# Kernel optimization log

Measured on AMD Instinct MI355X. Metric: run time of the kernel, lower is better.

The kernel has to match this reference:

```python
import jax, jax.numpy as jnp
import numpy as np

U, SI, TI = 100000, 50000, 40000
D = 64
B = 8192
NNZ_S, NNZ_T = 3_200_000, 2_560_000
P_DROP = 0.2


def setup_inputs() -> dict:
    key = jax.random.key(0)
    ks = iter(jax.random.split(key, 32))
    nxt = lambda: next(ks)
    emb = lambda n: (jax.random.normal(nxt(), (n, D), jnp.float32) * 0.1)
    keep = lambda n: jax.random.bernoulli(nxt(), 1.0 - P_DROP, (n,)).astype(jnp.float32) / (1.0 - P_DROP)
    inp = {}
    inp['user'] = jax.random.randint(nxt(), (B,), 0, U, jnp.int32)
    inp['source_pos_item'] = jax.random.randint(nxt(), (B,), 0, SI, jnp.int32)
    inp['source_neg_item'] = jax.random.randint(nxt(), (B,), 0, SI, jnp.int32)
    inp['target_pos_item'] = jax.random.randint(nxt(), (B,), 0, TI, jnp.int32)
    inp['target_neg_item'] = jax.random.randint(nxt(), (B,), 0, TI, jnp.int32)
    inp['mask_s'] = jax.random.bernoulli(nxt(), 0.5, (B,))
    inp['mask_t'] = jax.random.bernoulli(nxt(), 0.5, (B,))
    inp['su_int'] = emb(U); inp['si_int'] = emb(SI)
    inp['tu_int'] = emb(U); inp['ti_int'] = emb(TI)
    inp['su_pop'] = emb(U); inp['si_pop'] = emb(SI)
    inp['tu_pop'] = emb(U); inp['ti_pop'] = emb(TI)
    Ns, Nt = U + SI, U + TI
    inp['s_rows'] = jax.random.randint(nxt(), (NNZ_S,), 0, Ns, jnp.int32)
    inp['s_cols'] = jax.random.randint(nxt(), (NNZ_S,), 0, Ns, jnp.int32)
    inp['s_vals'] = jax.random.uniform(nxt(), (NNZ_S,), jnp.float32, 0.0, 0.02)
    inp['t_rows'] = jax.random.randint(nxt(), (NNZ_T,), 0, Nt, jnp.int32)
    inp['t_cols'] = jax.random.randint(nxt(), (NNZ_T,), 0, Nt, jnp.int32)
    inp['t_vals'] = jax.random.uniform(nxt(), (NNZ_T,), jnp.float32, 0.0, 0.02)
    inp['drop_s_int'] = keep(NNZ_S); inp['drop_t_int'] = keep(NNZ_T)
    inp['drop_s_pop'] = keep(NNZ_S); inp['drop_t_pop'] = keep(NNZ_T)
    return inp


def _lightgcn(emb, rows, cols, vals, n_users):
    # 1-layer LightGCN: out = mean([e0, A @ e0]) ; A given as COO (rows, cols, vals)
    agg = jax.ops.segment_sum(vals[:, None] * emb[cols], rows, num_segments=emb.shape[0])
    out = 0.5 * (emb + agg)
    return out[:n_users], out[n_users:]


def _bpr(p, n):
    return -jnp.mean(jax.nn.log_sigmoid(p - n))


def _mask_bpr(p, n, m):
    return -jnp.mean(m.astype(p.dtype) * jax.nn.log_sigmoid(p - n))


def _masked_l1(a, b, idx):
    # L1Loss(mean) over rows selected by unique(idx); membership mask avoids jnp.unique
    m = jnp.zeros((a.shape[0],), bool).at[idx].set(True)
    cnt = jnp.maximum(m.sum(), 1).astype(a.dtype)
    return jnp.sum(jnp.abs(a - b) * m[:, None]) / (cnt * a.shape[1])


def reference(user, source_pos_item, source_neg_item, target_pos_item, target_neg_item,
              mask_s, mask_t,
              su_int, si_int, tu_int, ti_int, su_pop, si_pop, tu_pop, ti_pop,
              s_rows, s_cols, s_vals, t_rows, t_cols, t_vals,
              drop_s_int, drop_t_int, drop_s_pop, drop_t_pop):
    # int factor
    us_i, is_i = _lightgcn(jnp.concatenate([su_int, si_int]), s_rows, s_cols, s_vals * drop_s_int, U)
    ut_i, it_i = _lightgcn(jnp.concatenate([tu_int, ti_int]), t_rows, t_cols, t_vals * drop_t_int, U)
    # pop factor
    us_p, is_p = _lightgcn(jnp.concatenate([su_pop, si_pop]), s_rows, s_cols, s_vals * drop_s_pop, U)
    ut_p, it_p = _lightgcn(jnp.concatenate([tu_pop, ti_pop]), t_rows, t_cols, t_vals * drop_t_pop, U)

    dot = lambda ue, ie, u, i: jnp.sum(ue[u] * ie[i], axis=1)
    sp_i = dot(us_i, is_i, user, source_pos_item); sn_i = dot(us_i, is_i, user, source_neg_item)
    sp_p = dot(us_p, is_p, user, source_pos_item); sn_p = dot(us_p, is_p, user, source_neg_item)
    tp_i = dot(ut_i, it_i, user, target_pos_item); tn_i = dot(ut_i, it_i, user, target_neg_item)
    tp_p = dot(ut_p, it_p, user, target_pos_item); tn_p = dot(ut_p, it_p, user, target_neg_item)

    loss_int_s = _mask_bpr(sp_i, sn_i, mask_s)
    loss_pop_s = _mask_bpr(sn_p, sp_p, mask_s) + _mask_bpr(sp_p, sn_p, ~mask_s)
    loss_int_t = _mask_bpr(tp_i, tn_i, mask_t)
    loss_pop_t = _mask_bpr(tn_p, tp_p, mask_t) + _mask_bpr(tp_p, tn_p, ~mask_t)
    loss_total_s = _bpr(sp_i + sp_p, sn_i + sn_p)
    loss_total_t = _bpr(tp_i + tp_p, tn_i + tn_p)

    item_all_s = jnp.concatenate([source_pos_item, source_neg_item])
    item_all_t = jnp.concatenate([target_pos_item, target_neg_item])
    dis_loss = (_masked_l1(su_int, su_pop, user) + _masked_l1(si_int, si_pop, item_all_s)
                + _masked_l1(tu_int, tu_pop, user) + _masked_l1(ti_int, ti_pop, item_all_t))

    loss = (loss_total_s + loss_total_t
            + 0.1 * (loss_int_s + loss_int_t)
            + 0.1 * (loss_pop_s + loss_pop_t)
            - 0.01 * dis_loss)
    return loss
```

## Files before the change

### kernel.cpp

```cpp
#include <hip/hip_runtime.h>
#include <math.h>

constexpr int U_N = 100000;
constexpr int SI_N = 50000;
constexpr int TI_N = 40000;
constexpr int D = 64;
constexpr int B = 8192;
constexpr int NS = U_N + SI_N;
constexpr int NT = U_N + TI_N;
constexpr int SLOTS = 3 * B;
constexpr int CAP = 64;
constexpr int OVCAP = 4096;
constexpr int NROWS_ALL = U_N + SI_N + TI_N;
constexpr int NCHUNK = (NROWS_ALL + 63) / 64;

__device__ __forceinline__ float wave_sum(float x) {
#pragma unroll
  for (int m = 32; m; m >>= 1) x += __shfl_xor(x, m, 64);
  return x;
}

__device__ __forceinline__ float softplus_f(float z) {
  return fmaxf(z, 0.f) + log1pf(expf(-fabsf(z)));
}

__global__ __launch_bounds__(256) void k_init(
    const int* __restrict__ user, const int* __restrict__ spos, const int* __restrict__ sneg,
    const int* __restrict__ tpos, const int* __restrict__ tneg,
    int* __restrict__ map_s, int* __restrict__ map_t,
    const unsigned char* __restrict__ m, int* __restrict__ det) {
  if (blockIdx.x < 96) {
    int t = blockIdx.x * blockDim.x + threadIdx.x;
    if (t < B) {
      int u = user[t];
      map_s[u] = t;
      map_t[u] = t;
    } else if (t < 2 * B) {
      int b = t - B;
      map_s[U_N + spos[b]] = t;
      map_t[U_N + tpos[b]] = t;
    } else {
      int b = t - 2 * B;
      map_s[U_N + sneg[b]] = t;
      map_t[U_N + tneg[b]] = t;
    }
    return;
  }
  int t = threadIdx.x;
  int cb = 0, cc = 0;
  for (int i = t; i < B; i += 256) {
    unsigned char v = m[i];
    if ((i & 3) && v) cb++;
    if (v > 1) cc++;
  }
#pragma unroll
  for (int off = 32; off; off >>= 1) {
    cb += __shfl_xor(cb, off, 64);
    cc += __shfl_xor(cc, off, 64);
  }
  __shared__ int sb[4], sc[4];
  if ((t & 63) == 0) { sb[t >> 6] = cb; sc[t >> 6] = cc; }
  __syncthreads();
  if (t == 0) {
    det[0] = sb[0] + sb[1] + sb[2] + sb[3];
    det[1] = sc[0] + sc[1] + sc[2] + sc[3];
  }
}

__global__ __launch_bounds__(256) void k_compact2(
    const int* __restrict__ s_rows, const int* __restrict__ t_rows,
    const int* __restrict__ map_s, const int* __restrict__ map_t,
    int* __restrict__ cnt_s, int* __restrict__ cnt_t,
    int* __restrict__ bucket_s, int* __restrict__ bucket_t,
    int* __restrict__ ovcnt_s, int* __restrict__ ovcnt_t,
    int* __restrict__ ov_s, int* __restrict__ ov_t, int nnz_s, int nnz_t) {
  int e = blockIdx.x * 256 + threadIdx.x;
  const int* rows;
  const int* map;
  int* cnt;
  int* bucket;
  int* ovcnt;
  int* ov;
  if (e < nnz_s) {
    rows = s_rows; map = map_s; cnt = cnt_s; bucket = bucket_s; ovcnt = ovcnt_s; ov = ov_s;
  } else {
    e -= nnz_s;
    if (e >= nnz_t) return;
    rows = t_rows; map = map_t; cnt = cnt_t; bucket = bucket_t; ovcnt = ovcnt_t; ov = ov_t;
  }
  int slot = map[rows[e]];
  if (slot < 0) return;
  int pos = atomicAdd(&cnt[slot], 1);
  if (pos < CAP) {
    bucket[slot * CAP + pos] = e;
  } else {
    int o = atomicAdd(ovcnt, 1);
    if (o < OVCAP) { ov[2 * o] = slot; ov[2 * o + 1] = e; }
  }
}

__device__ __forceinline__ void accum_slot(
    int s, int lane,
    const int* __restrict__ cols, const float* __restrict__ vals,
    const float* __restrict__ di, const float* __restrict__ dp,
    const int* __restrict__ cnt, const int* __restrict__ bucket,
    const int* __restrict__ ovcnt, const int* __restrict__ ov,
    const float* __restrict__ eu_i, const float* __restrict__ ei_i,
    const float* __restrict__ eu_p, const float* __restrict__ ei_p,
    float* __restrict__ aggA, float* __restrict__ aggB) {
  int m = min(cnt[s], CAP);
  int g = lane >> 4, sub = lane & 15;
  int c = 0;
  float wi = 0.f, wp = 0.f;
  if (lane < m) {
    int e = bucket[s * CAP + lane];
    c = cols[e];
    float v = vals[e];
    wi = v * di[e];
    wp = v * dp[e];
  }
  float aIx = 0, aIy = 0, aIz = 0, aIw = 0;
  float aPx = 0, aPy = 0, aPz = 0, aPw = 0;
  for (int k = 0; k < m; k += 16) {
    int i0 = k + g, i1 = k + 4 + g, i2 = k + 8 + g, i3 = k + 12 + g;
    int c0 = __shfl(c, i0, 64), c1 = __shfl(c, i1, 64);
    int c2 = __shfl(c, i2, 64), c3 = __shfl(c, i3, 64);
    float wi0 = __shfl(wi, i0, 64), wi1 = __shfl(wi, i1, 64);
    float wi2 = __shfl(wi, i2, 64), wi3 = __shfl(wi, i3, 64);
    float wp0 = __shfl(wp, i0, 64), wp1 = __shfl(wp, i1, 64);
    float wp2 = __shfl(wp, i2, 64), wp3 = __shfl(wp, i3, 64);
    const float* bi0 = (c0 < U_N) ? (eu_i + (size_t)c0 * D) : (ei_i + (size_t)(c0 - U_N) * D);
    const float* bi1 = (c1 < U_N) ? (eu_i + (size_t)c1 * D) : (ei_i + (size_t)(c1 - U_N) * D);
    const float* bi2 = (c2 < U_N) ? (eu_i + (size_t)c2 * D) : (ei_i + (size_t)(c2 - U_N) * D);
    const float* bi3 = (c3 < U_N) ? (eu_i + (size_t)c3 * D) : (ei_i + (size_t)(c3 - U_N) * D);
    const float* bp0 = (c0 < U_N) ? (eu_p + (size_t)c0 * D) : (ei_p + (size_t)(c0 - U_N) * D);
    const float* bp1 = (c1 < U_N) ? (eu_p + (size_t)c1 * D) : (ei_p + (size_t)(c1 - U_N) * D);
    const float* bp2 = (c2 < U_N) ? (eu_p + (size_t)c2 * D) : (ei_p + (size_t)(c2 - U_N) * D);
    const float* bp3 = (c3 < U_N) ? (eu_p + (size_t)c3 * D) : (ei_p + (size_t)(c3 - U_N) * D);
    float4 vI0 = *(const float4*)(bi0 + 4 * sub);
    float4 vI1 = *(const float4*)(bi1 + 4 * sub);
    float4 vI2 = *(const float4*)(bi2 + 4 * sub);
    float4 vI3 = *(const float4*)(bi3 + 4 * sub);
    float4 vP0 = *(const float4*)(bp0 + 4 * sub);
    float4 vP1 = *(const float4*)(bp1 + 4 * sub);
    float4 vP2 = *(const float4*)(bp2 + 4 * sub);
    float4 vP3 = *(const float4*)(bp3 + 4 * sub);
    aIx = fmaf(wi0, vI0.x, aIx); aIy = fmaf(wi0, vI0.y, aIy);
    aIz = fmaf(wi0, vI0.z, aIz); aIw = fmaf(wi0, vI0.w, aIw);
    aIx = fmaf(wi1, vI1.x, aIx); aIy = fmaf(wi1, vI1.y, aIy);
    aIz = fmaf(wi1, vI1.z, aIz); aIw = fmaf(wi1, vI1.w, aIw);
    aIx = fmaf(wi2, vI2.x, aIx); aIy = fmaf(wi2, vI2.y, aIy);
    aIz = fmaf(wi2, vI2.z, aIz); aIw = fmaf(wi2, vI2.w, aIw);
    aIx = fmaf(wi3, vI3.x, aIx); aIy = fmaf(wi3, vI3.y, aIy);
    aIz = fmaf(wi3, vI3.z, aIz); aIw = fmaf(wi3, vI3.w, aIw);
    aPx = fmaf(wp0, vP0.x, aPx); aPy = fmaf(wp0, vP0.y, aPy);
    aPz = fmaf(wp0, vP0.z, aPz); aPw = fmaf(wp0, vP0.w, aPw);
    aPx = fmaf(wp1, vP1.x, aPx); aPy = fmaf(wp1, vP1.y, aPy);
    aPz = fmaf(wp1, vP1.z, aPz); aPw = fmaf(wp1, vP1.w, aPw);
    aPx = fmaf(wp2, vP2.x, aPx); aPy = fmaf(wp2, vP2.y, aPy);
    aPz = fmaf(wp2, vP2.z, aPz); aPw = fmaf(wp2, vP2.w, aPw);
    aPx = fmaf(wp3, vP3.x, aPx); aPy = fmaf(wp3, vP3.y, aPy);
    aPz = fmaf(wp3, vP3.z, aPz); aPw = fmaf(wp3, vP3.w, aPw);
  }
#define XRED(x) x += __shfl_xor(x, 16, 64); x += __shfl_xor(x, 32, 64);
  XRED(aIx) XRED(aIy) XRED(aIz) XRED(aIw)
  XRED(aPx) XRED(aPy) XRED(aPz) XRED(aPw)
#undef XRED
  int nov = min(*ovcnt, OVCAP);
  for (int i = 0; i < nov; ++i) {
    if (ov[2 * i] == s) {
      int e = ov[2 * i + 1];
      int cc = cols[e];
      float v = vals[e];
      float wwi = v * di[e], wwp = v * dp[e];
      const float* bi = (cc < U_N) ? (eu_i + (size_t)cc * D) : (ei_i + (size_t)(cc - U_N) * D);
      const float* bp = (cc < U_N) ? (eu_p + (size_t)cc * D) : (ei_p + (size_t)(cc - U_N) * D);
      if (lane < 16) {
        float4 vI = *(const float4*)(bi + 4 * sub);
        float4 vP = *(const float4*)(bp + 4 * sub);
        aIx = fmaf(wwi, vI.x, aIx); aIy = fmaf(wwi, vI.y, aIy);
        aIz = fmaf(wwi, vI.z, aIz); aIw = fmaf(wwi, vI.w, aIw);
        aPx = fmaf(wwp, vP.x, aPx); aPy = fmaf(wwp, vP.y, aPy);
        aPz = fmaf(wwp, vP.z, aPz); aPw = fmaf(wwp, vP.w, aPw);
      }
    }
  }
  if (lane < 16) {
    *(float4*)(aggA + (size_t)s * D + 4 * sub) = make_float4(aIx, aIy, aIz, aIw);
    *(float4*)(aggB + (size_t)s * D + 4 * sub) = make_float4(aPx, aPy, aPz, aPw);
  }
}

__global__ __launch_bounds__(256) void k_accum_pair(
    const int* __restrict__ s_cols, const float* __restrict__ s_vals,
    const float* __restrict__ dsi, const float* __restrict__ dsp,
    const int* __restrict__ t_cols, const float* __restrict__ t_vals,
    const float* __restrict__ dti, const float* __restrict__ dtp,
    const int* __restrict__ cnt_s, const int* __restrict__ bucket_s,
    const int* __restrict__ ovcnt_s, const int* __restrict__ ov_s,
    const int* __restrict__ cnt_t, const int* __restrict__ bucket_t,
    const int* __restrict__ ovcnt_t, const int* __restrict__ ov_t,
    const float* __restrict__ su_i, const float* __restrict__ si_i,
    const float* __restrict__ su_p, const float* __restrict__ si_p,
    const float* __restrict__ tu_i, const float* __restrict__ ti_i,
    const float* __restrict__ tu_p, const float* __restrict__ ti_p,
    float* __restrict__ aggSA, float* __restrict__ aggSB,
    float* __restrict__ aggTA, float* __restrict__ aggTB) {
  int lane = threadIdx.x & 63;
  int sg = (blockIdx.x * 256 + threadIdx.x) >> 6;
  if (sg >= 2 * SLOTS) return;
  if (sg < SLOTS) {
    accum_slot(sg, lane, s_cols, s_vals, dsi, dsp, cnt_s, bucket_s, ovcnt_s, ov_s,
               su_i, si_i, su_p, si_p, aggSA, aggSB);
  } else {
    accum_slot(sg - SLOTS, lane, t_cols, t_vals, dti, dtp, cnt_t, bucket_t, ovcnt_t, ov_t,
               tu_i, ti_i, tu_p, ti_p, aggTA, aggTB);
  }
}

__global__ __launch_bounds__(256) void k_dots_loss(
    const int* __restrict__ user,
    const int* __restrict__ spos, const int* __restrict__ sneg,
    const int* __restrict__ tpos, const int* __restrict__ tneg,
    const unsigned char* __restrict__ ms8, const unsigned char* __restrict__ mt8,
    const int* __restrict__ det,
    const float* __restrict__ su_i, const float* __restrict__ si_i,
    const float* __restrict__ su_p, const float* __restrict__ si_p,
    const float* __restrict__ tu_i, const float* __restrict__ ti_i,
    const float* __restrict__ tu_p, const float* __restrict__ ti_p,
    const int* __restrict__ map_s, const int* __restrict__ map_t,
    const float* __restrict__ aggSA, const float* __restrict__ aggSB,
    const float* __restrict__ aggTA, const float* __restrict__ aggTB,
    float* __restrict__ acc) {
  int lane = threadIdx.x & 63;
  int b = (blockIdx.x * blockDim.x + threadIdx.x) >> 6;
  float contrib = 0.f;
  if (b < B) {
    int u = user[b];
    int ps = spos[b], ns = sneg[b], pt = tpos[b], nt = tneg[b];
    int sus = map_s[u], sps = map_s[U_N + ps], sns = map_s[U_N + ns];
    int sut = map_t[u], spt = map_t[U_N + pt], snt = map_t[U_N + nt];
    float oui = su_i[(size_t)u * D + lane] + aggSA[(size_t)sus * D + lane];
    float oup = su_p[(size_t)u * D + lane] + aggSB[(size_t)sus * D + lane];
    float opi = si_i[(size_t)ps * D + lane] + aggSA[(size_t)sps * D + lane];
    float opp = si_p[(size_t)ps * D + lane] + aggSB[(size_t)sps * D + lane];
    float oni = si_i[(size_t)ns * D + lane] + aggSA[(size_t)sns * D + lane];
    float onp = si_p[(size_t)ns * D + lane] + aggSB[(size_t)sns * D + lane];
    float spi = 0.25f * wave_sum(oui * opi);
    float sni = 0.25f * wave_sum(oui * oni);
    float spp = 0.25f * wave_sum(oup * opp);
    float snp = 0.25f * wave_sum(oup * onp);
    float tui = tu_i[(size_t)u * D + lane] + aggTA[(size_t)sut * D + lane];
    float tup = tu_p[(size_t)u * D + lane] + aggTB[(size_t)sut * D + lane];
    float tpi_ = ti_i[(size_t)pt * D + lane] + aggTA[(size_t)spt * D + lane];
    float tpp_ = ti_p[(size_t)pt * D + lane] + aggTB[(size_t)spt * D + lane];
    float tni_ = ti_i[(size_t)nt * D + lane] + aggTA[(size_t)snt * D + lane];
    float tnp_ = ti_p[(size_t)nt * D + lane] + aggTB[(size_t)snt * D + lane];
    float tpi = 0.25f * wave_sum(tui * tpi_);
    float tni = 0.25f * wave_sum(tui * tni_);
    float tpp = 0.25f * wave_sum(tup * tpp_);
    float tnp = 0.25f * wave_sum(tup * tnp_);
    int db = det[0], dc = det[1];
    float ms, mt;
    if (dc > 100) {
      ms = (((const float*)ms8)[b] != 0.f) ? 1.f : 0.f;
      mt = (((const float*)mt8)[b] != 0.f) ? 1.f : 0.f;
    } else if (db > 100) {
      ms = ms8[b] ? 1.f : 0.f;
      mt = mt8[b] ? 1.f : 0.f;
    } else {
      ms = ((const int*)ms8)[b] ? 1.f : 0.f;
      mt = ((const int*)mt8)[b] ? 1.f : 0.f;
    }
    float l_int_s = ms * softplus_f(sni - spi);
    float l_pop_s = ms * softplus_f(spp - snp) + (1.f - ms) * softplus_f(snp - spp);
    float l_tot_s = softplus_f((sni + snp) - (spi + spp));
    float l_int_t = mt * softplus_f(tni - tpi);
    float l_pop_t = mt * softplus_f(tpp - tnp) + (1.f - mt) * softplus_f(tnp - tpp);
    float l_tot_t = softplus_f((tni + tnp) - (tpi + tpp));
    contrib = (l_tot_s + l_tot_t + 0.1f * (l_int_s + l_int_t) +
               0.1f * (l_pop_s + l_pop_t)) * (1.f / (float)B);
  }
  __shared__ float wsum_[4];
  if (lane == 0) wsum_[threadIdx.x >> 6] = contrib;
  __syncthreads();
  if (threadIdx.x == 0) atomicAdd(&acc[0], wsum_[0] + wsum_[1] + wsum_[2] + wsum_[3]);
}

__global__ __launch_bounds__(256) void k_l1_final(
    const float* __restrict__ su_i, const float* __restrict__ su_p,
    const float* __restrict__ tu_i, const float* __restrict__ tu_p,
    const float* __restrict__ si_i, const float* __restrict__ si_p,
    const float* __restrict__ ti_i, const float* __restrict__ ti_p,
    const int* __restrict__ map_s, const int* __restrict__ map_t,
    float* __restrict__ acc, int* __restrict__ done_ctr,
    float* __restrict__ out) {
  int lane = threadIdx.x & 63;
  int wave = (blockIdx.x * blockDim.x + threadIdx.x) >> 6;
  int nwaves = (gridDim.x * blockDim.x) >> 6;
  float a1 = 0.f, a2 = 0.f, a3 = 0.f, a4 = 0.f;
  float c5 = 0.f, c6 = 0.f, c7 = 0.f;
  for (int ch = wave; ch < NCHUNK; ch += nwaves) {
    int r0 = ch * 64;
    int r = r0 + lane;
    int flag = -1;
    if (r < NROWS_ALL) flag = (r < NS) ? map_s[r] : map_t[r - SI_N];
    bool valid = flag >= 0;
    unsigned long long m0 = __ballot(valid && r < U_N);
    unsigned long long m1 = __ballot(valid && r >= U_N && r < NS);
    unsigned long long m2 = __ballot(valid && r >= NS);
    if (lane == 0) {
      c5 += (float)__popcll(m0);
      c6 += (float)__popcll(m1);
      c7 += (float)__popcll(m2);
    }
    unsigned long long mm = m0 | m1 | m2;
    while (mm) {
      int bit = __ffsll((unsigned long long)mm) - 1;
      mm &= mm - 1;
      int rr = r0 + bit;
      if (rr < U_N) {
        size_t o = (size_t)rr * D + lane;
        a1 += fabsf(su_i[o] - su_p[o]);
        a3 += fabsf(tu_i[o] - tu_p[o]);
      } else if (rr < NS) {
        size_t o = (size_t)(rr - U_N) * D + lane;
        a2 += fabsf(si_i[o] - si_p[o]);
      } else {
        size_t o = (size_t)(rr - NS) * D + lane;
        a4 += fabsf(ti_i[o] - ti_p[o]);
      }
    }
  }
  a1 = wave_sum(a1);
  a2 = wave_sum(a2);
  a3 = wave_sum(a3);
  a4 = wave_sum(a4);
  __shared__ float sb[4][8];
  if (lane == 0) {
    int w = threadIdx.x >> 6;
    sb[w][0] = a1; sb[w][1] = a2; sb[w][2] = a3; sb[w][3] = a4;
    sb[w][4] = c5; sb[w][5] = c6; sb[w][6] = c7;
  }
  __syncthreads();
  int t = threadIdx.x;
  if (t < 7) {
    float v = sb[0][t] + sb[1][t] + sb[2][t] + sb[3][t];
    atomicAdd(&acc[1 + t], v);
  }
  __syncthreads();
  if (t == 0) {
    __threadfence();
    int old = atomicAdd(done_ctr, 1);
    if (old == (int)gridDim.x - 1) {
      float a0 = atomicAdd(&acc[0], 0.f);
      float n1 = atomicAdd(&acc[1], 0.f);
      float n2 = atomicAdd(&acc[2], 0.f);
      float n3 = atomicAdd(&acc[3], 0.f);
      float n4 = atomicAdd(&acc[4], 0.f);
      float cu = fmaxf(atomicAdd(&acc[5], 0.f), 1.f);
      float cs = fmaxf(atomicAdd(&acc[6], 0.f), 1.f);
      float ct = fmaxf(atomicAdd(&acc[7], 0.f), 1.f);
      float dis = n1 / (cu * (float)D) + n2 / (cs * (float)D) +
                  n3 / (cu * (float)D) + n4 / (ct * (float)D);
      out[0] = a0 - 0.01f * dis;
    }
  }
}

extern "C" void kernel_launch(void* const* d_in, const int* in_sizes, int n_in,
                              void* d_out, int out_size, void* d_ws, size_t ws_size,
                              hipStream_t stream) {
  const int* user = (const int*)d_in[0];
  const int* spos = (const int*)d_in[1];
  const int* sneg = (const int*)d_in[2];
  const int* tpos = (const int*)d_in[3];
  const int* tneg = (const int*)d_in[4];
  const unsigned char* mask_s = (const unsigned char*)d_in[5];
  const unsigned char* mask_t = (const unsigned char*)d_in[6];
  const float* su_int = (const float*)d_in[7];
  const float* si_int = (const float*)d_in[8];
  const float* tu_int = (const float*)d_in[9];
  const float* ti_int = (const float*)d_in[10];
  const float* su_pop = (const float*)d_in[11];
  const float* si_pop = (const float*)d_in[12];
  const float* tu_pop = (const float*)d_in[13];
  const float* ti_pop = (const float*)d_in[14];
  const int* s_rows = (const int*)d_in[15];
  const int* s_cols = (const int*)d_in[16];
  const float* s_vals = (const float*)d_in[17];
  const int* t_rows = (const int*)d_in[18];
  const int* t_cols = (const int*)d_in[19];
  const float* t_vals = (const float*)d_in[20];
  const float* drop_s_int = (const float*)d_in[21];
  const float* drop_t_int = (const float*)d_in[22];
  const float* drop_s_pop = (const float*)d_in[23];
  const float* drop_t_pop = (const float*)d_in[24];
  const int nnz_s = in_sizes[15];
  const int nnz_t = in_sizes[18];

  float* acc = (float*)d_ws;
  int* done_ctr = (int*)(acc + 16);
  int* det = done_ctr + 1;
  int* ovcnt_s = det + 2;
  int* ovcnt_t = ovcnt_s + 1;
  int* cnt_s = ovcnt_t + 1;
  int* cnt_t = cnt_s + SLOTS;
  int* map_s = cnt_t + SLOTS;
  int* map_t = map_s + NS;
  int* ov_s = map_t + NT;
  int* ov_t = ov_s + 2 * OVCAP;
  int* bucket_s = ov_t + 2 * OVCAP;
  int* bucket_t = bucket_s + SLOTS * CAP;
  float* aggSA = (float*)(bucket_t + SLOTS * CAP);
  float* aggSB = aggSA + (size_t)SLOTS * D;
  float* aggTA = aggSB + (size_t)SLOTS * D;
  float* aggTB = aggTA + (size_t)SLOTS * D;

  hipMemsetAsync(acc, 0, (size_t)(16 + 1 + 2 + 2 + 2 * SLOTS) * sizeof(int), stream);
  hipMemsetAsync(map_s, 0xFF, (size_t)(NS + NT) * sizeof(int), stream);

  k_init<<<97, 256, 0, stream>>>(user, spos, sneg, tpos, tneg, map_s, map_t, mask_s, det);

  k_compact2<<<(nnz_s + nnz_t + 255) / 256, 256, 0, stream>>>(
      s_rows, t_rows, map_s, map_t, cnt_s, cnt_t, bucket_s, bucket_t,
      ovcnt_s, ovcnt_t, ov_s, ov_t, nnz_s, nnz_t);

  k_accum_pair<<<2 * SLOTS / 4, 256, 0, stream>>>(
      s_cols, s_vals, drop_s_int, drop_s_pop, t_cols, t_vals, drop_t_int, drop_t_pop,
      cnt_s, bucket_s, ovcnt_s, ov_s, cnt_t, bucket_t, ovcnt_t, ov_t,
      su_int, si_int, su_pop, si_pop, tu_int, ti_int, tu_pop, ti_pop,
      aggSA, aggSB, aggTA, aggTB);

  k_dots_loss<<<(B + 3) / 4, 256, 0, stream>>>(
      user, spos, sneg, tpos, tneg, mask_s, mask_t, det,
      su_int, si_int, su_pop, si_pop, tu_int, ti_int, tu_pop, ti_pop,
      map_s, map_t, aggSA, aggSB, aggTA, aggTB, acc);

  k_l1_final<<<768, 256, 0, stream>>>(su_int, su_pop, tu_int, tu_pop,
                                      si_int, si_pop, ti_int, ti_pop,
                                      map_s, map_t, acc, done_ctr, (float*)d_out);
}
```

Measured before the change: 483.8 us.

## Pack col and weights into buckets, shrink CAP, merge dots and L1 kernels

The compaction kernel now gathers each edge's column, value and both dropout weights once and stores them as an int4 in the bucket. This removes the dependent indirect loads through the edge index in the accumulation kernel. CAP drops from 64 to 48, trading more overflow-list traffic for smaller buckets. The dot-product/loss and L1 kernels are fused into one launch that shares a done-counter finalization, removing one kernel launch. Compact writes 16 bytes per kept edge instead of 4, and all edges beyond 48 per row now go through the serial overflow scan.

```diff
diff --git a/kernel.cpp b/kernel.cpp
--- a/kernel.cpp
+++ b/kernel.cpp
@@ -9,10 +9,12 @@
 constexpr int NS = U_N + SI_N;
 constexpr int NT = U_N + TI_N;
 constexpr int SLOTS = 3 * B;
-constexpr int CAP = 64;
+constexpr int CAP = 48;
 constexpr int OVCAP = 4096;
 constexpr int NROWS_ALL = U_N + SI_N + TI_N;
 constexpr int NCHUNK = (NROWS_ALL + 63) / 64;
+constexpr int DOTS_BLOCKS = B / 4;
+constexpr int L1_BLOCKS = 768;
 
 __device__ __forceinline__ float wave_sum(float x) {
 #pragma unroll
@@ -68,56 +70,72 @@
 }
 
 __global__ __launch_bounds__(256) void k_compact2(
-    const int* __restrict__ s_rows, const int* __restrict__ t_rows,
+    const int* __restrict__ s_rows, const int* __restrict__ s_cols,
+    const float* __restrict__ s_vals,
+    const float* __restrict__ dsi, const float* __restrict__ dsp,
+    const int* __restrict__ t_rows, const int* __restrict__ t_cols,
+    const float* __restrict__ t_vals,
+    const float* __restrict__ dti, const float* __restrict__ dtp,
     const int* __restrict__ map_s, const int* __restrict__ map_t,
     int* __restrict__ cnt_s, int* __restrict__ cnt_t,
-    int* __restrict__ bucket_s, int* __restrict__ bucket_t,
+    int4* __restrict__ bucket_s, int4* __restrict__ bucket_t,
     int* __restrict__ ovcnt_s, int* __restrict__ ovcnt_t,
-    int* __restrict__ ov_s, int* __restrict__ ov_t, int nnz_s, int nnz_t) {
+    int4* __restrict__ ov_s, int4* __restrict__ ov_t, int nnz_s, int nnz_t) {
   int e = blockIdx.x * 256 + threadIdx.x;
   const int* rows;
+  const int* cols;
+  const float* vals;
+  const float* di;
+  const float* dp;
   const int* map;
   int* cnt;
-  int* bucket;
+  int4* bucket;
   int* ovcnt;
-  int* ov;
+  int4* ov;
   if (e < nnz_s) {
-    rows = s_rows; map = map_s; cnt = cnt_s; bucket = bucket_s; ovcnt = ovcnt_s; ov = ov_s;
+    rows = s_rows; cols = s_cols; vals = s_vals; di = dsi; dp = dsp;
+    map = map_s; cnt = cnt_s; bucket = bucket_s; ovcnt = ovcnt_s; ov = ov_s;
   } else {
     e -= nnz_s;
     if (e >= nnz_t) return;
-    rows = t_rows; map = map_t; cnt = cnt_t; bucket = bucket_t; ovcnt = ovcnt_t; ov = ov_t;
+    rows = t_rows; cols = t_cols; vals = t_vals; di = dti; dp = dtp;
+    map = map_t; cnt = cnt_t; bucket = bucket_t; ovcnt = ovcnt_t; ov = ov_t;
   }
   int slot = map[rows[e]];
   if (slot < 0) return;
+  float v = vals[e];
+  float wi = v * di[e];
+  float wp = v * dp[e];
+  int c = cols[e];
   int pos = atomicAdd(&cnt[slot], 1);
   if (pos < CAP) {
-    bucket[slot * CAP + pos] = e;
+    bucket[(size_t)slot * CAP + pos] =
+        make_int4(c, __float_as_int(wi), __float_as_int(wp), 0);
   } else {
     int o = atomicAdd(ovcnt, 1);
-    if (o < OVCAP) { ov[2 * o] = slot; ov[2 * o + 1] = e; }
+    if (o < OVCAP) {
+      ov[o] = make_int4(slot, c, __float_as_int(wi), __float_as_int(wp));
+    }
   }
 }
 
 __device__ __forceinline__ void accum_slot(
     int s, int lane,
-    const int* __restrict__ cols, const float* __restrict__ vals,
-    const float* __restrict__ di, const float* __restrict__ dp,
-    const int* __restrict__ cnt, const int* __restrict__ bucket,
-    const int* __restrict__ ovcnt, const int* __restrict__ ov,
+    const int* __restrict__ cnt, const int4* __restrict__ bucket,
+    const int* __restrict__ ovcnt, const int4* __restrict__ ov,
     const float* __restrict__ eu_i, const float* __restrict__ ei_i,
     const float* __restrict__ eu_p, const float* __restrict__ ei_p,
     float* __restrict__ aggA, float* __restrict__ aggB) {
+  int li = min(lane, CAP - 1);
+  int4 pl = bucket[(size_t)s * CAP + li];
   int m = min(cnt[s], CAP);
   int g = lane >> 4, sub = lane & 15;
   int c = 0;
   float wi = 0.f, wp = 0.f;
   if (lane < m) {
-    int e = bucket[s * CAP + lane];
-    c = cols[e];
-    float v = vals[e];
-    wi = v * di[e];
-    wp = v * dp[e];
+    c = pl.x;
+    wi = __int_as_float(pl.y);
+    wp = __int_as_float(pl.z);
   }
   float aIx = 0, aIy = 0, aIz = 0, aIw = 0;
   float aPx = 0, aPy = 0, aPz = 0, aPw = 0;
@@ -168,11 +186,10 @@
 #undef XRED
   int nov = min(*ovcnt, OVCAP);
   for (int i = 0; i < nov; ++i) {
-    if (ov[2 * i] == s) {
-      int e = ov[2 * i + 1];
-      int cc = cols[e];
-      float v = vals[e];
-      float wwi = v * di[e], wwp = v * dp[e];
+    int4 q = ov[i];
+    if (q.x == s) {
+      int cc = q.y;
+      float wwi = __int_as_float(q.z), wwp = __int_as_float(q.w);
       const float* bi = (cc < U_N) ? (eu_i + (size_t)cc * D) : (ei_i + (size_t)(cc - U_N) * D);
       const float* bp = (cc < U_N) ? (eu_p + (size_t)cc * D) : (ei_p + (size_t)(cc - U_N) * D);
       if (lane < 16) {
@@ -192,14 +209,10 @@
 }
 
 __global__ __launch_bounds__(256) void k_accum_pair(
-    const int* __restrict__ s_cols, const float* __restrict__ s_vals,
-    const float* __restrict__ dsi, const float* __restrict__ dsp,
-    const int* __restrict__ t_cols, const float* __restrict__ t_vals,
-    const float* __restrict__ dti, const float* __restrict__ dtp,
-    const int* __restrict__ cnt_s, const int* __restrict__ bucket_s,
-    const int* __restrict__ ovcnt_s, const int* __restrict__ ov_s,
-    const int* __restrict__ cnt_t, const int* __restrict__ bucket_t,
-    const int* __restrict__ ovcnt_t, const int* __restrict__ ov_t,
+    const int* __restrict__ cnt_s, const int4* __restrict__ bucket_s,
+    const int* __restrict__ ovcnt_s, const int4* __restrict__ ov_s,
+    const int* __restrict__ cnt_t, const int4* __restrict__ bucket_t,
+    const int* __restrict__ ovcnt_t, const int4* __restrict__ ov_t,
     const float* __restrict__ su_i, const float* __restrict__ si_i,
     const float* __restrict__ su_p, const float* __restrict__ si_p,
     const float* __restrict__ tu_i, const float* __restrict__ ti_i,
@@ -210,15 +223,36 @@
   int sg = (blockIdx.x * 256 + threadIdx.x) >> 6;
   if (sg >= 2 * SLOTS) return;
   if (sg < SLOTS) {
-    accum_slot(sg, lane, s_cols, s_vals, dsi, dsp, cnt_s, bucket_s, ovcnt_s, ov_s,
+    accum_slot(sg, lane, cnt_s, bucket_s, ovcnt_s, ov_s,
                su_i, si_i, su_p, si_p, aggSA, aggSB);
   } else {
-    accum_slot(sg - SLOTS, lane, t_cols, t_vals, dti, dtp, cnt_t, bucket_t, ovcnt_t, ov_t,
+    accum_slot(sg - SLOTS, lane, cnt_t, bucket_t, ovcnt_t, ov_t,
                tu_i, ti_i, tu_p, ti_p, aggTA, aggTB);
   }
 }
 
-__global__ __launch_bounds__(256) void k_dots_loss(
+__device__ __forceinline__ void finish_block(float* __restrict__ acc,
+                                             int* __restrict__ done_ctr,
+                                             float* __restrict__ out,
+                                             int nblocks) {
+  __threadfence();
+  int old = atomicAdd(done_ctr, 1);
+  if (old == nblocks - 1) {
+    float a0 = atomicAdd(&acc[0], 0.f);
+    float n1 = atomicAdd(&acc[1], 0.f);
+    float n2 = atomicAdd(&acc[2], 0.f);
+    float n3 = atomicAdd(&acc[3], 0.f);
+    float n4 = atomicAdd(&acc[4], 0.f);
+    float cu = fmaxf(atomicAdd(&acc[5], 0.f), 1.f);
+    float cs = fmaxf(atomicAdd(&acc[6], 0.f), 1.f);
+    float ct = fmaxf(atomicAdd(&acc[7], 0.f), 1.f);
+    float dis = n1 / (cu * (float)D) + n2 / (cs * (float)D) +
+                n3 / (cu * (float)D) + n4 / (ct * (float)D);
+    out[0] = a0 - 0.01f * dis;
+  }
+}
+
+__global__ __launch_bounds__(256) void k_tail(
     const int* __restrict__ user,
     const int* __restrict__ spos, const int* __restrict__ sneg,
     const int* __restrict__ tpos, const int* __restrict__ tneg,
@@ -231,73 +265,69 @@
     const int* __restrict__ map_s, const int* __restrict__ map_t,
     const float* __restrict__ aggSA, const float* __restrict__ aggSB,
     const float* __restrict__ aggTA, const float* __restrict__ aggTB,
-    float* __restrict__ acc) {
-  int lane = threadIdx.x & 63;
-  int b = (blockIdx.x * blockDim.x + threadIdx.x) >> 6;
-  float contrib = 0.f;
-  if (b < B) {
-    int u = user[b];
-    int ps = spos[b], ns = sneg[b], pt = tpos[b], nt = tneg[b];
-    int sus = map_s[u], sps = map_s[U_N + ps], sns = map_s[U_N + ns];
-    int sut = map_t[u], spt = map_t[U_N + pt], snt = map_t[U_N + nt];
-    float oui = su_i[(size_t)u * D + lane] + aggSA[(size_t)sus * D + lane];
-    float oup = su_p[(size_t)u * D + lane] + aggSB[(size_t)sus * D + lane];
-    float opi = si_i[(size_t)ps * D + lane] + aggSA[(size_t)sps * D + lane];
-    float opp = si_p[(size_t)ps * D + lane] + aggSB[(size_t)sps * D + lane];
-    float oni = si_i[(size_t)ns * D + lane] + aggSA[(size_t)sns * D + lane];
-    float onp = si_p[(size_t)ns * D + lane] + aggSB[(size_t)sns * D + lane];
-    float spi = 0.25f * wave_sum(oui * opi);
-    float sni = 0.25f * wave_sum(oui * oni);
-    float spp = 0.25f * wave_sum(oup * opp);
-    float snp = 0.25f * wave_sum(oup * onp);
-    float tui = tu_i[(size_t)u * D + lane] + aggTA[(size_t)sut * D + lane];
-    float tup = tu_p[(size_t)u * D + lane] + aggTB[(size_t)sut * D + lane];
-    float tpi_ = ti_i[(size_t)pt * D + lane] + aggTA[(size_t)spt * D + lane];
-    float tpp_ = ti_p[(size_t)pt * D + lane] + aggTB[(size_t)spt * D + lane];
-    float tni_ = ti_i[(size_t)nt * D + lane] + aggTA[(size_t)snt * D + lane];
-    float tnp_ = ti_p[(size_t)nt * D + lane] + aggTB[(size_t)snt * D + lane];
-    float tpi = 0.25f * wave_sum(tui * tpi_);
-    float tni = 0.25f * wave_sum(tui * tni_);
-    float tpp = 0.25f * wave_sum(tup * tpp_);
-    float tnp = 0.25f * wave_sum(tup * tnp_);
-    int db = det[0], dc = det[1];
-    float ms, mt;
-    if (dc > 100) {
-      ms = (((const float*)ms8)[b] != 0.f) ? 1.f : 0.f;
-      mt = (((const float*)mt8)[b] != 0.f) ? 1.f : 0.f;
-    } else if (db > 100) {
-      ms = ms8[b] ? 1.f : 0.f;
-      mt = mt8[b] ? 1.f : 0.f;
-    } else {
-      ms = ((const int*)ms8)[b] ? 1.f : 0.f;
-      mt = ((const int*)mt8)[b] ? 1.f : 0.f;
-    }
-    float l_int_s = ms * softplus_f(sni - spi);
-    float l_pop_s = ms * softplus_f(spp - snp) + (1.f - ms) * softplus_f(snp - spp);
-    float l_tot_s = softplus_f((sni + snp) - (spi + spp));
-    float l_int_t = mt * softplus_f(tni - tpi);
-    float l_pop_t = mt * softplus_f(tpp - tnp) + (1.f - mt) * softplus_f(tnp - tpp);
-    float l_tot_t = softplus_f((tni + tnp) - (tpi + tpp));
-    contrib = (l_tot_s + l_tot_t + 0.1f * (l_int_s + l_int_t) +
-               0.1f * (l_pop_s + l_pop_t)) * (1.f / (float)B);
-  }
-  __shared__ float wsum_[4];
-  if (lane == 0) wsum_[threadIdx.x >> 6] = contrib;
-  __syncthreads();
-  if (threadIdx.x == 0) atomicAdd(&acc[0], wsum_[0] + wsum_[1] + wsum_[2] + wsum_[3]);
-}
-
-__global__ __launch_bounds__(256) void k_l1_final(
-    const float* __restrict__ su_i, const float* __restrict__ su_p,
-    const float* __restrict__ tu_i, const float* __restrict__ tu_p,
-    const float* __restrict__ si_i, const float* __restrict__ si_p,
-    const float* __restrict__ ti_i, const float* __restrict__ ti_p,
-    const int* __restrict__ map_s, const int* __restrict__ map_t,
     float* __restrict__ acc, int* __restrict__ done_ctr,
     float* __restrict__ out) {
   int lane = threadIdx.x & 63;
-  int wave = (blockIdx.x * blockDim.x + threadIdx.x) >> 6;
-  int nwaves = (gridDim.x * blockDim.x) >> 6;
+  if (blockIdx.x < DOTS_BLOCKS) {
+    int b = (blockIdx.x * blockDim.x + threadIdx.x) >> 6;
+    float contrib = 0.f;
+    if (b < B) {
+      int u = user[b];
+      int ps = spos[b], ns = sneg[b], pt = tpos[b], nt = tneg[b];
+      int sus = map_s[u], sps = map_s[U_N + ps], sns = map_s[U_N + ns];
+      int sut = map_t[u], spt = map_t[U_N + pt], snt = map_t[U_N + nt];
+      float oui = su_i[(size_t)u * D + lane] + aggSA[(size_t)sus * D + lane];
+      float oup = su_p[(size_t)u * D + lane] + aggSB[(size_t)sus * D + lane];
+      float opi = si_i[(size_t)ps * D + lane] + aggSA[(size_t)sps * D + lane];
+      float opp = si_p[(size_t)ps * D + lane] + aggSB[(size_t)sps * D + lane];
+      float oni = si_i[(size_t)ns * D + lane] + aggSA[(size_t)sns * D + lane];
+      float onp = si_p[(size_t)ns * D + lane] + aggSB[(size_t)sns * D + lane];
+      float spi = 0.25f * wave_sum(oui * opi);
+      float sni = 0.25f * wave_sum(oui * oni);
+      float spp = 0.25f * wave_sum(oup * opp);
+      float snp = 0.25f * wave_sum(oup * onp);
+      float tui = tu_i[(size_t)u * D + lane] + aggTA[(size_t)sut * D + lane];
+      float tup = tu_p[(size_t)u * D + lane] + aggTB[(size_t)sut * D + lane];
+      float tpi_ = ti_i[(size_t)pt * D + lane] + aggTA[(size_t)spt * D + lane];
+      float tpp_ = ti_p[(size_t)pt * D + lane] + aggTB[(size_t)spt * D + lane];
+      float tni_ = ti_i[(size_t)nt * D + lane] + aggTA[(size_t)snt * D + lane];
+      float tnp_ = ti_p[(size_t)nt * D + lane] + aggTB[(size_t)snt * D + lane];
+      float tpi = 0.25f * wave_sum(tui * tpi_);
+      float tni = 0.25f * wave_sum(tui * tni_);
+      float tpp = 0.25f * wave_sum(tup * tpp_);
+      float tnp = 0.25f * wave_sum(tup * tnp_);
+      int db = det[0], dc = det[1];
+      float ms, mt;
+      if (dc > 100) {
+        ms = (((const float*)ms8)[b] != 0.f) ? 1.f : 0.f;
+        mt = (((const float*)mt8)[b] != 0.f) ? 1.f : 0.f;
+      } else if (db > 100) {
+        ms = ms8[b] ? 1.f : 0.f;
+        mt = mt8[b] ? 1.f : 0.f;
+      } else {
+        ms = ((const int*)ms8)[b] ? 1.f : 0.f;
+        mt = ((const int*)mt8)[b] ? 1.f : 0.f;
+      }
+      float l_int_s = ms * softplus_f(sni - spi);
+      float l_pop_s = ms * softplus_f(spp - snp) + (1.f - ms) * softplus_f(snp - spp);
+      float l_tot_s = softplus_f((sni + snp) - (spi + spp));
+      float l_int_t = mt * softplus_f(tni - tpi);
+      float l_pop_t = mt * softplus_f(tpp - tnp) + (1.f - mt) * softplus_f(tnp - tpp);
+      float l_tot_t = softplus_f((tni + tnp) - (tpi + tpp));
+      contrib = (l_tot_s + l_tot_t + 0.1f * (l_int_s + l_int_t) +
+                 0.1f * (l_pop_s + l_pop_t)) * (1.f / (float)B);
+    }
+    __shared__ float wsum_[4];
+    if (lane == 0) wsum_[threadIdx.x >> 6] = contrib;
+    __syncthreads();
+    if (threadIdx.x == 0) {
+      atomicAdd(&acc[0], wsum_[0] + wsum_[1] + wsum_[2] + wsum_[3]);
+      finish_block(acc, done_ctr, out, (int)gridDim.x);
+    }
+    return;
+  }
+  int wave = ((blockIdx.x - DOTS_BLOCKS) * blockDim.x + threadIdx.x) >> 6;
+  int nwaves = (L1_BLOCKS * 256) >> 6;
   float a1 = 0.f, a2 = 0.f, a3 = 0.f, a4 = 0.f;
   float c5 = 0.f, c6 = 0.f, c7 = 0.f;
   for (int ch = wave; ch < NCHUNK; ch += nwaves) {
@@ -349,23 +379,7 @@
     atomicAdd(&acc[1 + t], v);
   }
   __syncthreads();
-  if (t == 0) {
-    __threadfence();
-    int old = atomicAdd(done_ctr, 1);
-    if (old == (int)gridDim.x - 1) {
-      float a0 = atomicAdd(&acc[0], 0.f);
-      float n1 = atomicAdd(&acc[1], 0.f);
-      float n2 = atomicAdd(&acc[2], 0.f);
-      float n3 = atomicAdd(&acc[3], 0.f);
-      float n4 = atomicAdd(&acc[4], 0.f);
-      float cu = fmaxf(atomicAdd(&acc[5], 0.f), 1.f);
-      float cs = fmaxf(atomicAdd(&acc[6], 0.f), 1.f);
-      float ct = fmaxf(atomicAdd(&acc[7], 0.f), 1.f);
-      float dis = n1 / (cu * (float)D) + n2 / (cs * (float)D) +
-                  n3 / (cu * (float)D) + n4 / (ct * (float)D);
-      out[0] = a0 - 0.01f * dis;
-    }
-  }
+  if (t == 0) finish_block(acc, done_ctr, out, (int)gridDim.x);
 }
 
 extern "C" void kernel_launch(void* const* d_in, const int* in_sizes, int n_in,
@@ -399,7 +413,15 @@
   const int nnz_s = in_sizes[15];
   const int nnz_t = in_sizes[18];
 
-  float* acc = (float*)d_ws;
+  int4* bucket_s = (int4*)d_ws;
+  int4* bucket_t = bucket_s + (size_t)SLOTS * CAP;
+  int4* ov_s = bucket_t + (size_t)SLOTS * CAP;
+  int4* ov_t = ov_s + OVCAP;
+  float* aggSA = (float*)(ov_t + OVCAP);
+  float* aggSB = aggSA + (size_t)SLOTS * D;
+  float* aggTA = aggSB + (size_t)SLOTS * D;
+  float* aggTB = aggTA + (size_t)SLOTS * D;
+  float* acc = aggTB + (size_t)SLOTS * D;
   int* done_ctr = (int*)(acc + 16);
   int* det = done_ctr + 1;
   int* ovcnt_s = det + 2;
@@ -408,14 +430,6 @@
   int* cnt_t = cnt_s + SLOTS;
   int* map_s = cnt_t + SLOTS;
   int* map_t = map_s + NS;
-  int* ov_s = map_t + NT;
-  int* ov_t = ov_s + 2 * OVCAP;
-  int* bucket_s = ov_t + 2 * OVCAP;
-  int* bucket_t = bucket_s + SLOTS * CAP;
-  float* aggSA = (float*)(bucket_t + SLOTS * CAP);
-  float* aggSB = aggSA + (size_t)SLOTS * D;
-  float* aggTA = aggSB + (size_t)SLOTS * D;
-  float* aggTB = aggTA + (size_t)SLOTS * D;
 
   hipMemsetAsync(acc, 0, (size_t)(16 + 1 + 2 + 2 + 2 * SLOTS) * sizeof(int), stream);
   hipMemsetAsync(map_s, 0xFF, (size_t)(NS + NT) * sizeof(int), stream);
@@ -423,21 +437,19 @@
   k_init<<<97, 256, 0, stream>>>(user, spos, sneg, tpos, tneg, map_s, map_t, mask_s, det);
 
   k_compact2<<<(nnz_s + nnz_t + 255) / 256, 256, 0, stream>>>(
-      s_rows, t_rows, map_s, map_t, cnt_s, cnt_t, bucket_s, bucket_t,
+      s_rows, s_cols, s_vals, drop_s_int, drop_s_pop,
+      t_rows, t_cols, t_vals, drop_t_int, drop_t_pop,
+      map_s, map_t, cnt_s, cnt_t, bucket_s, bucket_t,
       ovcnt_s, ovcnt_t, ov_s, ov_t, nnz_s, nnz_t);
 
   k_accum_pair<<<2 * SLOTS / 4, 256, 0, stream>>>(
-      s_cols, s_vals, drop_s_int, drop_s_pop, t_cols, t_vals, drop_t_int, drop_t_pop,
       cnt_s, bucket_s, ovcnt_s, ov_s, cnt_t, bucket_t, ovcnt_t, ov_t,
       su_int, si_int, su_pop, si_pop, tu_int, ti_int, tu_pop, ti_pop,
       aggSA, aggSB, aggTA, aggTB);
 
-  k_dots_loss<<<(B + 3) / 4, 256, 0, stream>>>(
+  k_tail<<<DOTS_BLOCKS + L1_BLOCKS, 256, 0, stream>>>(
       user, spos, sneg, tpos, tneg, mask_s, mask_t, det,
       su_int, si_int, su_pop, si_pop, tu_int, ti_int, tu_pop, ti_pop,
-      map_s, map_t, aggSA, aggSB, aggTA, aggTB, acc);
-
-  k_l1_final<<<768, 256, 0, stream>>>(su_int, su_pop, tu_int, tu_pop,
-                                      si_int, si_pop, ti_int, ti_pop,
-                                      map_s, map_t, acc, done_ctr, (float*)d_out);
-}
+      map_s, map_t, aggSA, aggSB, aggTA, aggTB,
+      acc, done_ctr, (float*)d_out);
+}
```

Result: no change. 475.6 us (-1.7%).
